# Kernel optimization log

Measured on AMD Instinct MI355X. Metric: run time of the kernel, lower is better.

## Reference

```python
import jax, jax.numpy as jnp
import numpy as np

B, N, F_IN, K, NUM_CLASSES = 16, 2048, 8, 35, 4
EPS = 1e-5


def _bn(x, g, b):
    # BatchNorm in training mode: stats over all leading (batch/node/edge) dims.
    ax = tuple(range(x.ndim - 1))
    mu = jnp.mean(x, axis=ax, keepdims=True)
    var = jnp.var(x, axis=ax, keepdims=True)
    return g * (x - mu) * jax.lax.rsqrt(var + EPS) + b


def _edge_feats(h, k):
    # h: [B,N,C]. Dynamic kNN within each graph (self included, as torch_cluster.knn),
    # then EdgeConv features cat([x_i, x_j - x_i]) -> [B,N,k,2C].
    sq = jnp.sum(h * h, -1)                                   # [B,N]
    d = sq[:, :, None] + sq[:, None, :] - 2.0 * jnp.einsum('bnc,bmc->bnm', h, h)
    _, idx = jax.lax.top_k(-d, k)                             # [B,N,k]
    hj = jax.vmap(lambda hb, ib: hb[ib])(h, idx)              # [B,N,k,C]
    hi = jnp.broadcast_to(h[:, :, None, :], hj.shape)
    return jnp.concatenate([hi, hj - hi], axis=-1)


def _forward(x, w1, b1, g1, bt1, w2, b2, g2, bt2, w3, b3, w4, b4,
             w5, b5, w6, b6, g6, bt6, w7, b7, g7, bt7, w8, b8):
    # conv1: DynamicEdgeConv(MLP([16,64,64,64]), k, 'max'); plain_last => 3rd linear bare
    e = _edge_feats(x, K)                                     # [B,N,K,16]
    h = jax.nn.relu(_bn(e @ w1 + b1, g1, bt1))
    h = jax.nn.relu(_bn(h @ w2 + b2, g2, bt2))
    h = h @ w3 + b3
    x1 = jnp.max(h, axis=2)                                   # [B,N,64] scatter-max over k
    # conv2: DynamicEdgeConv(MLP([128,128]), k, 'max'); single plain linear
    e2 = _edge_feats(x1, K)                                   # [B,N,K,128]
    x2 = jnp.max(e2 @ w4 + b4, axis=2)                        # [B,N,128]
    out = jnp.concatenate([x1, x2], axis=-1) @ w5 + b5        # [B,N,256]
    pooled = jnp.max(out, axis=1)                             # [B,256] global_max_pool
    # head MLP([256,128,64,4], dropout eval-mode, batch_norm), plain_last
    h = jax.nn.relu(_bn(pooled @ w6 + b6, g6, bt6))
    h = jax.nn.relu(_bn(h @ w7 + b7, g7, bt7))
    return h @ w8 + b8                                        # [B,4]


def setup_inputs() -> dict:
    key = jax.random.key(0)
    ks = jax.random.split(key, 12)

    def lin(kk, fi, fo):
        k1, k2 = jax.random.split(kk)
        w = jax.random.normal(k1, (fi, fo), jnp.float32) / np.sqrt(fi).astype(np.float32)
        b = jax.random.normal(k2, (fo,), jnp.float32) * 0.01
        return w, b

    x = jax.random.normal(ks[0], (B, N, F_IN), jnp.float32)
    w1, b1 = lin(ks[1], 2 * F_IN, 64)
    w2, b2 = lin(ks[2], 64, 64)
    w3, b3 = lin(ks[3], 64, 64)
    w4, b4 = lin(ks[4], 2 * 64, 128)
    w5, b5 = lin(ks[5], 128 + 64, 256)
    w6, b6 = lin(ks[6], 256, 128)
    w7, b7 = lin(ks[7], 128, 64)
    w8, b8 = lin(ks[8], 64, NUM_CLASSES)
    ones, zeros = jnp.ones, jnp.zeros
    return {
        'x': x,
        'w1': w1, 'b1': b1, 'g1': ones(64), 'bt1': zeros(64),
        'w2': w2, 'b2': b2, 'g2': ones(64), 'bt2': zeros(64),
        'w3': w3, 'b3': b3,
        'w4': w4, 'b4': b4,
        'w5': w5, 'b5': b5,
        'w6': w6, 'b6': b6, 'g6': ones(128), 'bt6': zeros(128),
        'w7': w7, 'b7': b7, 'g7': ones(64), 'bt7': zeros(64),
        'w8': w8, 'b8': b8,
    }


def reference(x, w1, b1, g1, bt1, w2, b2, g2, bt2, w3, b3, w4, b4,
              w5, b5, w6, b6, g6, bt6, w7, b7, g7, bt7, w8, b8):
    return _forward(x, w1, b1, g1, bt1, w2, b2, g2, bt2, w3, b3, w4, b4,
                    w5, b5, w6, b6, g6, bt6, w7, b7, g7, bt7, w8, b8)
```

## Files before the change

kernel.cpp:

```cpp
#include <hip/hip_runtime.h>
#include <cfloat>
#include <cstdint>

constexpr int Bn   = 16;
constexpr int Nn   = 2048;
constexpr int Fin  = 8;
constexpr int Kn   = 35;
constexpr int NODES = Bn * Nn;
constexpr int EDG   = NODES * Kn;
constexpr int NSTATB = 1024;
constexpr float EPSV = 1e-5f;

typedef _Float16 f16;
typedef _Float16 f16x2 __attribute__((ext_vector_type(2)));

__device__ __forceinline__ unsigned enc_f(float f){
    unsigned u = __float_as_uint(f);
    return (u & 0x80000000u) ? ~u : (u | 0x80000000u);
}
__device__ __forceinline__ float dec_f(unsigned e){
    unsigned u = (e & 0x80000000u) ? (e ^ 0x80000000u) : ~e;
    return __uint_as_float(u);
}

template<int C>
__global__ __launch_bounds__(256) void sq_kernel(const float* __restrict__ h, float* __restrict__ sq){
    int i = blockIdx.x * 256 + threadIdx.x;
    if (i >= NODES) return;
    const float* p = h + (size_t)i * C;
    float s = 0.f;
#pragma unroll
    for (int c = 0; c < C; c++) s += p[c] * p[c];
    sq[i] = s;
}

template<int C>
__global__ __launch_bounds__(256) void knn_kernel(const float* __restrict__ h, const float* __restrict__ sq,
                                                  int* __restrict__ idxout){
    __shared__ float dist[4][Nn];
    __shared__ float hi4[4][C];
    __shared__ float sqi[4];
    __shared__ float statred[4][3][4];
    __shared__ unsigned long long keybuf[4][128];
    int t  = threadIdx.x;
    int b  = blockIdx.x >> 9;
    int i0 = (blockIdx.x & 511) * 4;
    int w  = t >> 6, lane = t & 63;

    for (int i = t; i < 4 * C; i += 256)
        hi4[i / C][i % C] = h[((size_t)(b * Nn) + i0 + i / C) * C + (i % C)];
    if (t < 4) sqi[t] = sq[b * Nn + i0 + t];
    __syncthreads();

    const float4* H0 = (const float4*)hi4[0];
    const float4* H1 = (const float4*)hi4[1];
    const float4* H2 = (const float4*)hi4[2];
    const float4* H3 = (const float4*)hi4[3];
    float ps0=0.f,ps1=0.f,ps2=0.f,ps3=0.f, pq0=0.f,pq1=0.f,pq2=0.f,pq3=0.f;
    float mn0=FLT_MAX,mn1=FLT_MAX,mn2=FLT_MAX,mn3=FLT_MAX;
    for (int j = t; j < Nn; j += 256){
        const float4* hj = (const float4*)(h + ((size_t)(b * Nn) + j) * C);
        float d0 = 0.f, d1 = 0.f, d2 = 0.f, d3 = 0.f;
#pragma unroll 4
        for (int c4 = 0; c4 < C / 4; c4++){
            float4 v = hj[c4];
            float4 a0 = H0[c4], a1 = H1[c4], a2 = H2[c4], a3 = H3[c4];
            d0 += a0.x*v.x + a0.y*v.y + a0.z*v.z + a0.w*v.w;
            d1 += a1.x*v.x + a1.y*v.y + a1.z*v.z + a1.w*v.w;
            d2 += a2.x*v.x + a2.y*v.y + a2.z*v.z + a2.w*v.w;
            d3 += a3.x*v.x + a3.y*v.y + a3.z*v.z + a3.w*v.w;
        }
        float sj = sq[b * Nn + j];
        float D0 = sqi[0] + sj - 2.f*d0; dist[0][j] = D0; ps0 += D0; pq0 += D0*D0; mn0 = fminf(mn0, D0);
        float D1 = sqi[1] + sj - 2.f*d1; dist[1][j] = D1; ps1 += D1; pq1 += D1*D1; mn1 = fminf(mn1, D1);
        float D2 = sqi[2] + sj - 2.f*d2; dist[2][j] = D2; ps2 += D2; pq2 += D2*D2; mn2 = fminf(mn2, D2);
        float D3 = sqi[3] + sj - 2.f*d3; dist[3][j] = D3; ps3 += D3; pq3 += D3*D3; mn3 = fminf(mn3, D3);
    }
#pragma unroll
    for (int d = 1; d < 64; d <<= 1){
        ps0 += __shfl_xor(ps0, d); pq0 += __shfl_xor(pq0, d); mn0 = fminf(mn0, __shfl_xor(mn0, d));
        ps1 += __shfl_xor(ps1, d); pq1 += __shfl_xor(pq1, d); mn1 = fminf(mn1, __shfl_xor(mn1, d));
        ps2 += __shfl_xor(ps2, d); pq2 += __shfl_xor(pq2, d); mn2 = fminf(mn2, __shfl_xor(mn2, d));
        ps3 += __shfl_xor(ps3, d); pq3 += __shfl_xor(pq3, d); mn3 = fminf(mn3, __shfl_xor(mn3, d));
    }
    if (lane == 0){
        statred[0][0][w] = ps0; statred[0][1][w] = pq0; statred[0][2][w] = mn0;
        statred[1][0][w] = ps1; statred[1][1][w] = pq1; statred[1][2][w] = mn1;
        statred[2][0][w] = ps2; statred[2][1][w] = pq2; statred[2][2][w] = mn2;
        statred[3][0][w] = ps3; statred[3][1][w] = pq3; statred[3][2][w] = mn3;
    }
    __syncthreads();

    const float* dw = dist[w];
    float smu = statred[w][0][0] + statred[w][0][1] + statred[w][0][2] + statred[w][0][3];
    float mnq = fminf(fminf(statred[w][2][0], statred[w][2][1]),
                      fminf(statred[w][2][2], statred[w][2][3]));
    float mu = smu * (1.f / (float)Nn);
    float span = fmaxf(mu - mnq, 0.f);

    float lo = mnq;  int clo = 0;
    float hi = FLT_MAX;  int chi = Nn;

    float PV[5] = { mnq + 0.25f*span, mnq + 0.40f*span, mnq + 0.55f*span,
                    mnq + 0.75f*span, mu };
    int c0 = 0, c1 = 0, c2 = 0, c3 = 0, c4 = 0;
    for (int s8 = 0; s8 < 32; s8 += 8){
        float vv[8];
#pragma unroll
        for (int u = 0; u < 8; u++) vv[u] = dw[(s8 + u) * 64 + lane];
#pragma unroll
        for (int u = 0; u < 8; u++){
            float v = vv[u];
            c0 += (v < PV[0]) ? 1 : 0;
            c1 += (v < PV[1]) ? 1 : 0;
            c2 += (v < PV[2]) ? 1 : 0;
            c3 += (v < PV[3]) ? 1 : 0;
            c4 += (v < PV[4]) ? 1 : 0;
        }
    }
#pragma unroll
    for (int d = 1; d < 64; d <<= 1){
        c0 += __shfl_xor(c0, d);
        c1 += __shfl_xor(c1, d);
        c2 += __shfl_xor(c2, d);
        c3 += __shfl_xor(c3, d);
        c4 += __shfl_xor(c4, d);
    }
    {
        int CC[5] = {c0, c1, c2, c3, c4};
#pragma unroll
        for (int pi = 0; pi < 5; pi++){
            if (CC[pi] >= Kn){ if (PV[pi] < hi){ hi = PV[pi]; chi = CC[pi]; } }
            else             { if (PV[pi] > lo){ lo = PV[pi]; clo = CC[pi]; } }
        }
    }

    for (int it = 0; it < 24 && chi > 128; it++){
        int den = (chi - clo) > 0 ? (chi - clo) : 1;
        float piv = (it & 1) ? 0.5f * (lo + hi)
                             : lo + (hi - lo) * ((float)(96 - clo) / (float)den);
        if (!(piv > lo && piv < hi)) piv = 0.5f * (lo + hi);
        if (!(piv > lo && piv < hi)) break;
        int c = 0;
        for (int s8 = 0; s8 < 32; s8 += 8){
            float vv[8];
#pragma unroll
            for (int u = 0; u < 8; u++) vv[u] = dw[(s8 + u) * 64 + lane];
#pragma unroll
            for (int u = 0; u < 8; u++) c += (vv[u] < piv) ? 1 : 0;
        }
#pragma unroll
        for (int d = 1; d < 64; d <<= 1) c += __shfl_xor(c, d);
        if (c >= Kn){ hi = piv; chi = c; } else { lo = piv; clo = c; }
    }

    size_t obase = ((size_t)(b * Nn) + i0 + w) * Kn;

    if (chi <= 128){
        keybuf[w][lane]      = ~0ull;
        keybuf[w][lane + 64] = ~0ull;
        unsigned long long me_lower = (1ull << lane) - 1ull;
        int boff = 0;
        for (int s8 = 0; s8 < 32; s8 += 8){
            float vv[8];
#pragma unroll
            for (int u = 0; u < 8; u++) vv[u] = dw[(s8 + u) * 64 + lane];
#pragma unroll
            for (int u = 0; u < 8; u++){
                bool cnd = vv[u] < hi;
                unsigned long long m = __ballot(cnd);
                if (cnd){
                    int o = boff + __popcll(m & me_lower);
                    keybuf[w][o] = (((unsigned long long)enc_f(vv[u])) << 16) | (unsigned)((s8 + u) * 64 + lane);
                }
                boff += __popcll(m);
            }
        }
        unsigned long long k0 = keybuf[w][lane];
        unsigned long long k1 = keybuf[w][lane + 64];
        int r0 = 0, r1 = 0;
        int nR = (chi + 7) & ~7;
        for (int j2 = 0; j2 < nR; j2 += 8){
            unsigned long long a0 = keybuf[w][j2+0], a1 = keybuf[w][j2+1];
            unsigned long long a2 = keybuf[w][j2+2], a3 = keybuf[w][j2+3];
            unsigned long long a4 = keybuf[w][j2+4], a5 = keybuf[w][j2+5];
            unsigned long long a6 = keybuf[w][j2+6], a7 = keybuf[w][j2+7];
            r0 += (a0<k0)+(a1<k0)+(a2<k0)+(a3<k0)+(a4<k0)+(a5<k0)+(a6<k0)+(a7<k0);
            r1 += (a0<k1)+(a1<k1)+(a2<k1)+(a3<k1)+(a4<k1)+(a5<k1)+(a6<k1)+(a7<k1);
        }
        if (lane < chi      && r0 < Kn) idxout[obase + r0] = (int)(k0 & 0xffffu);
        if (lane + 64 < chi && r1 < Kn) idxout[obase + r1] = (int)(k1 & 0xffffu);
    } else {
        unsigned selmask = 0u;
        for (int e = 0; e < Kn; e++){
            unsigned long long best = ~0ull;
#pragma unroll
            for (int s = 0; s < 32; s++){
                float v = dw[s * 64 + lane];
                if (v < hi && !((selmask >> s) & 1)){
                    unsigned long long key = (((unsigned long long)enc_f(v)) << 16) | (unsigned)(s * 64 + lane);
                    best = (key < best) ? key : best;
                }
            }
#pragma unroll
            for (int d = 1; d < 64; d <<= 1){
                unsigned long long ov = __shfl_xor(best, d);
                best = (ov < best) ? ov : best;
            }
            int jj = (int)(best & 0xffffu);
            if ((jj & 63) == lane) selmask |= 1u << (jj >> 6);
            if (lane == 0) idxout[obase + e] = jj;
        }
    }
}

__global__ __launch_bounds__(256) void pre1_kernel(const float* __restrict__ x,
        const float* __restrict__ w1, const float* __restrict__ b1,
        float* __restrict__ p, float* __restrict__ q){
    int t = threadIdx.x, w = t >> 6, c = t & 63;
    float wd[8], wb[8];
#pragma unroll
    for (int f = 0; f < 8; f++){
        float wbv = w1[(8 + f) * 64 + c];
        wb[f] = wbv;
        wd[f] = w1[f * 64 + c] - wbv;
    }
    float b1c = b1[c];
    int slot = blockIdx.x * 4 + w;
    for (int it = 0; it < 16; it++){
        int node = slot + it * 2048;
        const float* xp = x + (size_t)node * Fin;
        float pv = b1c, qv = 0.f;
#pragma unroll
        for (int f = 0; f < 8; f++){
            float xv = xp[f];
            pv += xv * wd[f]; qv += xv * wb[f];
        }
        p[(size_t)node * 64 + c] = pv;
        q[(size_t)node * 64 + c] = qv;
    }
}

__global__ __launch_bounds__(256) void stats1_kernel(const float* __restrict__ p, const float* __restrict__ q,
        const int* __restrict__ idx, float* __restrict__ sumP, float* __restrict__ ssqP){
    __shared__ float red[2][4][64];
    int t = threadIdx.x, w = t >> 6, c = t & 63;
    float s = 0.f, ss = 0.f;
    int slot = blockIdx.x * 4 + w;
    for (int it = 0; it < 8; it++){
        int node = slot + it * 4096;
        int b = node >> 11;
        float pc = p[(size_t)node * 64 + c];
        const int* ip = idx + (size_t)node * Kn;
        for (int k = 0; k < Kn; k++){
            int j = ip[k];
            float z = pc + q[((size_t)(b << 11) + j) * 64 + c];
            s += z; ss += z * z;
        }
    }
    red[0][w][c] = s; red[1][w][c] = ss;
    __syncthreads();
    if (w == 0){
        sumP[blockIdx.x * 64 + c] = red[0][0][c] + red[0][1][c] + red[0][2][c] + red[0][3][c];
        ssqP[blockIdx.x * 64 + c] = red[1][0][c] + red[1][1][c] + red[1][2][c] + red[1][3][c];
    }
}

__global__ void finalize_kernel(const float* __restrict__ sumP, const float* __restrict__ ssqP,
        const float* __restrict__ gg, const float* __restrict__ bt,
        float* __restrict__ scale, float* __restrict__ shift, float inv_count){
    int c = threadIdx.x;
    float s = 0.f, q = 0.f;
    for (int i = 0; i < NSTATB; i++){ s += sumP[i * 64 + c]; q += ssqP[i * 64 + c]; }
    float mu  = s * inv_count;
    float var = q * inv_count - mu * mu;
    float sc  = gg[c] / sqrtf(var + EPSV);
    scale[c] = sc;
    shift[c] = bt[c] - mu * sc;
}

__global__ __launch_bounds__(256) void stats2_kernel(const float* __restrict__ p, const float* __restrict__ q,
        const int* __restrict__ idx,
        const float* __restrict__ sc1v, const float* __restrict__ sh1v,
        const float* __restrict__ w2, const float* __restrict__ b2,
        float* __restrict__ sumP, float* __restrict__ ssqP){
    __shared__ __align__(16) f16 hsh[4][2][64];
    __shared__ float red[2][4][64];
    int t = threadIdx.x, w = t >> 6, c = t & 63;
    f16x2 w2h[32];
#pragma unroll
    for (int f2 = 0; f2 < 32; f2++)
        w2h[f2] = f16x2{(f16)w2[(2*f2)*64 + c], (f16)w2[(2*f2+1)*64 + c]};
    float sc1 = sc1v[c], sh1 = sh1v[c], b2c = b2[c];
    float s = 0.f, ss = 0.f;
    int slot = blockIdx.x * 4 + w;
    for (int it = 0; it < 8; it++){
        int node = slot + it * 4096;
        int b = node >> 11;
        float pc = p[(size_t)node * 64 + c];
        const int* ip = idx + (size_t)node * Kn;
        for (int k = 0; k < Kn; k += 2){
            bool two = (k + 1 < Kn);
            int j0 = ip[k];
            int j1 = ip[two ? k + 1 : k];
            float za = pc + q[((size_t)(b << 11) + j0) * 64 + c];
            float zb = pc + q[((size_t)(b << 11) + j1) * 64 + c];
            hsh[w][0][c] = (f16)fmaxf(0.f, za * sc1 + sh1);
            hsh[w][1][c] = (f16)fmaxf(0.f, zb * sc1 + sh1);
            const uint4* h40 = (const uint4*)hsh[w][0];
            const uint4* h41 = (const uint4*)hsh[w][1];
            float p00=0.f,p01=0.f,p02=0.f,p03=0.f, p10=0.f,p11=0.f,p12=0.f,p13=0.f;
#pragma unroll
            for (int i = 0; i < 8; i++){
                uint4 u0 = h40[i], u1 = h41[i];
                p00 = __builtin_amdgcn_fdot2(__builtin_bit_cast(f16x2, u0.x), w2h[4*i+0], p00, false);
                p10 = __builtin_amdgcn_fdot2(__builtin_bit_cast(f16x2, u1.x), w2h[4*i+0], p10, false);
                p01 = __builtin_amdgcn_fdot2(__builtin_bit_cast(f16x2, u0.y), w2h[4*i+1], p01, false);
                p11 = __builtin_amdgcn_fdot2(__builtin_bit_cast(f16x2, u1.y), w2h[4*i+1], p11, false);
                p02 = __builtin_amdgcn_fdot2(__builtin_bit_cast(f16x2, u0.z), w2h[4*i+2], p02, false);
                p12 = __builtin_amdgcn_fdot2(__builtin_bit_cast(f16x2, u1.z), w2h[4*i+2], p12, false);
                p03 = __builtin_amdgcn_fdot2(__builtin_bit_cast(f16x2, u0.w), w2h[4*i+3], p03, false);
                p13 = __builtin_amdgcn_fdot2(__builtin_bit_cast(f16x2, u1.w), w2h[4*i+3], p13, false);
            }
            float z20 = b2c + ((p00 + p01) + (p02 + p03));
            float z21 = b2c + ((p10 + p11) + (p12 + p13));
            s += z20; ss += z20 * z20;
            if (two){ s += z21; ss += z21 * z21; }
        }
    }
    red[0][w][c] = s; red[1][w][c] = ss;
    __syncthreads();
    if (w == 0){
        sumP[blockIdx.x * 64 + c] = red[0][0][c] + red[0][1][c] + red[0][2][c] + red[0][3][c];
        ssqP[blockIdx.x * 64 + c] = red[1][0][c] + red[1][1][c] + red[1][2][c] + red[1][3][c];
    }
}

__global__ __launch_bounds__(256) void conv1_kernel(const float* __restrict__ p, const float* __restrict__ q,
        const int* __restrict__ idx,
        const float* __restrict__ sc1v, const float* __restrict__ sh1v,
        const float* __restrict__ w2, const float* __restrict__ b2,
        const float* __restrict__ sc2v, const float* __restrict__ sh2v,
        const float* __restrict__ w3, const float* __restrict__ b3,
        float* __restrict__ x1){
    __shared__ __align__(16) f16 hA[4][2][64];
    __shared__ __align__(16) f16 hB[4][2][64];
    int t = threadIdx.x, w = t >> 6, c = t & 63;
    f16x2 w2h[32], w3h[32];
#pragma unroll
    for (int f2 = 0; f2 < 32; f2++){
        w2h[f2] = f16x2{(f16)w2[(2*f2)*64 + c], (f16)w2[(2*f2+1)*64 + c]};
        w3h[f2] = f16x2{(f16)w3[(2*f2)*64 + c], (f16)w3[(2*f2+1)*64 + c]};
    }
    float sc1 = sc1v[c], sh1 = sh1v[c], sc2 = sc2v[c], sh2 = sh2v[c];
    float b2c = b2[c], b3c = b3[c];
    int node = blockIdx.x * 4 + w;
    int b = node >> 11;
    float pc = p[(size_t)node * 64 + c];
    const int* ip = idx + (size_t)node * Kn;
    float acc = -FLT_MAX;
    for (int k = 0; k < Kn; k += 2){
        bool two = (k + 1 < Kn);
        int j0 = ip[k];
        int j1 = ip[two ? k + 1 : k];
        float za = pc + q[((size_t)(b << 11) + j0) * 64 + c];
        float zb = pc + q[((size_t)(b << 11) + j1) * 64 + c];
        hA[w][0][c] = (f16)fmaxf(0.f, za * sc1 + sh1);
        hA[w][1][c] = (f16)fmaxf(0.f, zb * sc1 + sh1);
        const uint4* h40 = (const uint4*)hA[w][0];
        const uint4* h41 = (const uint4*)hA[w][1];
        float p00=0.f,p01=0.f,p02=0.f,p03=0.f, p10=0.f,p11=0.f,p12=0.f,p13=0.f;
#pragma unroll
        for (int i = 0; i < 8; i++){
            uint4 u0 = h40[i], u1 = h41[i];
            p00 = __builtin_amdgcn_fdot2(__builtin_bit_cast(f16x2, u0.x), w2h[4*i+0], p00, false);
            p10 = __builtin_amdgcn_fdot2(__builtin_bit_cast(f16x2, u1.x), w2h[4*i+0], p10, false);
            p01 = __builtin_amdgcn_fdot2(__builtin_bit_cast(f16x2, u0.y), w2h[4*i+1], p01, false);
            p11 = __builtin_amdgcn_fdot2(__builtin_bit_cast(f16x2, u1.y), w2h[4*i+1], p11, false);
            p02 = __builtin_amdgcn_fdot2(__builtin_bit_cast(f16x2, u0.z), w2h[4*i+2], p02, false);
            p12 = __builtin_amdgcn_fdot2(__builtin_bit_cast(f16x2, u1.z), w2h[4*i+2], p12, false);
            p03 = __builtin_amdgcn_fdot2(__builtin_bit_cast(f16x2, u0.w), w2h[4*i+3], p03, false);
            p13 = __builtin_amdgcn_fdot2(__builtin_bit_cast(f16x2, u1.w), w2h[4*i+3], p13, false);
        }
        float z20 = b2c + ((p00 + p01) + (p02 + p03));
        float z21 = b2c + ((p10 + p11) + (p12 + p13));
        hB[w][0][c] = (f16)fmaxf(0.f, z20 * sc2 + sh2);
        hB[w][1][c] = (f16)fmaxf(0.f, z21 * sc2 + sh2);
        const uint4* g40 = (const uint4*)hB[w][0];
        const uint4* g41 = (const uint4*)hB[w][1];
        float q00=0.f,q01=0.f,q02=0.f,q03=0.f, q10=0.f,q11=0.f,q12=0.f,q13=0.f;
#pragma unroll
        for (int i = 0; i < 8; i++){
            uint4 u0 = g40[i], u1 = g41[i];
            q00 = __builtin_amdgcn_fdot2(__builtin_bit_cast(f16x2, u0.x), w3h[4*i+0], q00, false);
            q10 = __builtin_amdgcn_fdot2(__builtin_bit_cast(f16x2, u1.x), w3h[4*i+0], q10, false);
            q01 = __builtin_amdgcn_fdot2(__builtin_bit_cast(f16x2, u0.y), w3h[4*i+1], q01, false);
            q11 = __builtin_amdgcn_fdot2(__builtin_bit_cast(f16x2, u1.y), w3h[4*i+1], q11, false);
            q02 = __builtin_amdgcn_fdot2(__builtin_bit_cast(f16x2, u0.z), w3h[4*i+2], q02, false);
            q12 = __builtin_amdgcn_fdot2(__builtin_bit_cast(f16x2, u1.z), w3h[4*i+2], q12, false);
            q03 = __builtin_amdgcn_fdot2(__builtin_bit_cast(f16x2, u0.w), w3h[4*i+3], q03, false);
            q13 = __builtin_amdgcn_fdot2(__builtin_bit_cast(f16x2, u1.w), w3h[4*i+3], q13, false);
        }
        float z30 = b3c + ((q00 + q01) + (q02 + q03));
        float z31 = b3c + ((q10 + q11) + (q12 + q13));
        acc = fmaxf(acc, z30);
        if (two) acc = fmaxf(acc, z31);
    }
    x1[(size_t)node * 64 + c] = acc;
}

__global__ __launch_bounds__(256) void pre2_kernel(const float* __restrict__ x1,
        const float* __restrict__ w4, const float* __restrict__ b4,
        float* __restrict__ u, float* __restrict__ v){
    __shared__ float x1s[16][64];
    int t = threadIdx.x;
    int c = t & 127, h = t >> 7;
    float wd[64], wb[64];
#pragma unroll
    for (int f = 0; f < 64; f++){
        float wbv = w4[(64 + f) * 128 + c];
        wb[f] = wbv;
        wd[f] = w4[f * 128 + c] - wbv;
    }
    float b4c = b4[c];
    int base = blockIdx.x * 16;
    for (int i = t; i < 16 * 64; i += 256)
        x1s[i >> 6][i & 63] = x1[(size_t)(base + (i >> 6)) * 64 + (i & 63)];
    __syncthreads();
    for (int n = 0; n < 8; n++){
        int node = base + h * 8 + n;
        const float4* xr = (const float4*)x1s[h * 8 + n];
        float u0 = 0.f, u1 = 0.f, v0 = 0.f, v1 = 0.f;
#pragma unroll
        for (int f4 = 0; f4 < 16; f4++){
            float4 xv = xr[f4];
            float pa = xv.x * wd[4*f4] + xv.y * wd[4*f4+1] + xv.z * wd[4*f4+2] + xv.w * wd[4*f4+3];
            float pb = xv.x * wb[4*f4] + xv.y * wb[4*f4+1] + xv.z * wb[4*f4+2] + xv.w * wb[4*f4+3];
            if (f4 & 1){ u1 += pa; v1 += pb; } else { u0 += pa; v0 += pb; }
        }
        u[(size_t)node * 128 + c] = b4c + u0 + u1;
        v[(size_t)node * 128 + c] = v0 + v1;
    }
}

__global__ __launch_bounds__(256) void gmax2_kernel(const float* __restrict__ v, const int* __restrict__ idx,
        float* __restrict__ x2){
    int t = threadIdx.x, g = t >> 7, c = t & 127;
    int node = blockIdx.x * 2 + g;
    int b = node >> 11;
    const int* ip = idx + (size_t)node * Kn;
    float vm = -FLT_MAX;
    for (int k = 0; k < Kn; k++){
        int j = ip[k];
        vm = fmaxf(vm, v[((size_t)(b << 11) + j) * 128 + c]);
    }
    x2[(size_t)node * 128 + c] += vm;
}

__global__ __launch_bounds__(256) void outpool_kernel(const float* __restrict__ x1, const float* __restrict__ x2,
        const float* __restrict__ w5, const float* __restrict__ b5, unsigned* __restrict__ pooled){
    __shared__ float rows[8][192];
    int t = threadIdx.x;
    int node0 = blockIdx.x * 8;
    for (int i = t; i < 8 * 192; i += 256){
        int e = i / 192, f = i - e * 192;
        int nd = node0 + e;
        rows[e][f] = (f < 64) ? x1[(size_t)nd * 64 + f] : x2[(size_t)nd * 128 + f - 64];
    }
    __syncthreads();
    float z[8];
#pragma unroll
    for (int e = 0; e < 8; e++) z[e] = b5[t];
    for (int f = 0; f < 192; f++){
        float w = w5[f * 256 + t];
#pragma unroll
        for (int e = 0; e < 8; e++) z[e] += rows[e][f] * w;
    }
    float m = z[0];
#pragma unroll
    for (int e = 1; e < 8; e++) m = fmaxf(m, z[e]);
    int b = node0 >> 11;
    atomicMax(&pooled[b * 256 + t], enc_f(m));
}

__global__ __launch_bounds__(256) void head_kernel(const unsigned* __restrict__ pooledE,
        const float* __restrict__ w6, const float* __restrict__ b6, const float* __restrict__ g6, const float* __restrict__ bt6,
        const float* __restrict__ w7, const float* __restrict__ b7, const float* __restrict__ g7, const float* __restrict__ bt7,
        const float* __restrict__ w8, const float* __restrict__ b8, float* __restrict__ out){
    __shared__ float P[16][256];
    __shared__ float H6[16][128];
    __shared__ float H7[16][64];
    int t = threadIdx.x;
    for (int i = t; i < 16 * 256; i += 256) P[i >> 8][i & 255] = dec_f(pooledE[i]);
    __syncthreads();
    for (int i = t; i < 16 * 128; i += 256){
        int r = i >> 7, c = i & 127;
        float z = b6[c];
        for (int f = 0; f < 256; f++) z += P[r][f] * w6[f * 128 + c];
        H6[r][c] = z;
    }
    __syncthreads();
    if (t < 128){
        float s = 0.f, q = 0.f;
        for (int r = 0; r < 16; r++){ float v = H6[r][t]; s += v; q += v * v; }
        float mu = s * (1.f / 16.f);
        float var = q * (1.f / 16.f) - mu * mu;
        float sc = g6[t] / sqrtf(var + EPSV);
        float sh = bt6[t] - mu * sc;
        for (int r = 0; r < 16; r++) H6[r][t] = fmaxf(0.f, H6[r][t] * sc + sh);
    }
    __syncthreads();
    for (int i = t; i < 16 * 64; i += 256){
        int r = i >> 6, c = i & 63;
        float z = b7[c];
        for (int f = 0; f < 128; f++) z += H6[r][f] * w7[f * 64 + c];
        H7[r][c] = z;
    }
    __syncthreads();
    if (t < 64){
        float s = 0.f, q = 0.f;
        for (int r = 0; r < 16; r++){ float v = H7[r][t]; s += v; q += v * v; }
        float mu = s * (1.f / 16.f);
        float var = q * (1.f / 16.f) - mu * mu;
        float sc = g7[t] / sqrtf(var + EPSV);
        float sh = bt7[t] - mu * sc;
        for (int r = 0; r < 16; r++) H7[r][t] = fmaxf(0.f, H7[r][t] * sc + sh);
    }
    __syncthreads();
    if (t < 64){
        int r = t >> 2, c = t & 3;
        float z = b8[c];
        for (int f = 0; f < 64; f++) z += H7[r][f] * w8[f * 4 + c];
        out[t] = z;
    }
}

extern "C" void kernel_launch(void* const* d_in, const int* in_sizes, int n_in,
                              void* d_out, int out_size, void* d_ws, size_t ws_size,
                              hipStream_t stream){
    const float* x   = (const float*)d_in[0];
    const float* w1  = (const float*)d_in[1];
    const float* b1  = (const float*)d_in[2];
    const float* g1  = (const float*)d_in[3];
    const float* bt1 = (const float*)d_in[4];
    const float* w2  = (const float*)d_in[5];
    const float* b2  = (const float*)d_in[6];
    const float* g2  = (const float*)d_in[7];
    const float* bt2 = (const float*)d_in[8];
    const float* w3  = (const float*)d_in[9];
    const float* b3  = (const float*)d_in[10];
    const float* w4  = (const float*)d_in[11];
    const float* b4  = (const float*)d_in[12];
    const float* w5  = (const float*)d_in[13];
    const float* b5  = (const float*)d_in[14];
    const float* w6  = (const float*)d_in[15];
    const float* b6  = (const float*)d_in[16];
    const float* g6  = (const float*)d_in[17];
    const float* bt6 = (const float*)d_in[18];
    const float* w7  = (const float*)d_in[19];
    const float* b7  = (const float*)d_in[20];
    const float* g7  = (const float*)d_in[21];
    const float* bt7 = (const float*)d_in[22];
    const float* w8  = (const float*)d_in[23];
    const float* b8  = (const float*)d_in[24];
    float* out = (float*)d_out;

    char* ws = (char*)d_ws;
    size_t off = 0;
    auto alloc = [&](size_t bytes)->char*{
        char* p = ws + off;
        off += (bytes + 255) & ~(size_t)255;
        return p;
    };
    int*      idx1   = (int*)alloc((size_t)EDG * 4);
    int*      idx2   = (int*)alloc((size_t)EDG * 4);
    float*    sq1    = (float*)alloc((size_t)NODES * 4);
    float*    sq2    = (float*)alloc((size_t)NODES * 4);
    float*    x1     = (float*)alloc((size_t)NODES * 64 * 4);
    float*    x2     = (float*)alloc((size_t)NODES * 128 * 4);
    float*    sumP   = (float*)alloc((size_t)NSTATB * 64 * 4);
    float*    ssqP   = (float*)alloc((size_t)NSTATB * 64 * 4);
    float*    scale1 = (float*)alloc(64 * 4);
    float*    shift1 = (float*)alloc(64 * 4);
    float*    scale2 = (float*)alloc(64 * 4);
    float*    shift2 = (float*)alloc(64 * 4);
    unsigned* pooled = (unsigned*)alloc((size_t)Bn * 256 * 4);
    float*    p      = (float*)alloc((size_t)NODES * 64 * 4);
    float*    q      = (float*)alloc((size_t)NODES * 64 * 4);
    float*    v      = p;

    hipMemsetAsync(pooled, 0, (size_t)Bn * 256 * 4, stream);

    sq_kernel<8><<<(NODES + 255) / 256, 256, 0, stream>>>(x, sq1);
    knn_kernel<8><<<NODES / 4, 256, 0, stream>>>(x, sq1, idx1);
    pre1_kernel<<<512, 256, 0, stream>>>(x, w1, b1, p, q);
    stats1_kernel<<<NSTATB, 256, 0, stream>>>(p, q, idx1, sumP, ssqP);
    finalize_kernel<<<1, 64, 0, stream>>>(sumP, ssqP, g1, bt1, scale1, shift1, 1.0f / (float)EDG);
    stats2_kernel<<<NSTATB, 256, 0, stream>>>(p, q, idx1, scale1, shift1, w2, b2, sumP, ssqP);
    finalize_kernel<<<1, 64, 0, stream>>>(sumP, ssqP, g2, bt2, scale2, shift2, 1.0f / (float)EDG);
    conv1_kernel<<<NODES / 4, 256, 0, stream>>>(p, q, idx1, scale1, shift1,
                                                w2, b2, scale2, shift2, w3, b3, x1);
    sq_kernel<64><<<(NODES + 255) / 256, 256, 0, stream>>>(x1, sq2);
    knn_kernel<64><<<NODES / 4, 256, 0, stream>>>(x1, sq2, idx2);
    pre2_kernel<<<NODES / 16, 256, 0, stream>>>(x1, w4, b4, x2, v);
    gmax2_kernel<<<NODES / 2, 256, 0, stream>>>(v, idx2, x2);
    outpool_kernel<<<NODES / 8, 256, 0, stream>>>(x1, x2, w5, b5, pooled);
    head_kernel<<<1, 256, 0, stream>>>(pooled, w6, b6, g6, bt6, w7, b7, g7, bt7, w8, b8, out);
}
```

Before: 1.335 ms.

## Split each kNN query row across two wavefronts with 512-thread blocks

After: 1.387 ms. 1.04x slower.

```diff
diff --git a/kernel.cpp b/kernel.cpp
--- a/kernel.cpp
+++ b/kernel.cpp
@@ -35,19 +35,20 @@
 }
 
 template<int C>
-__global__ __launch_bounds__(256) void knn_kernel(const float* __restrict__ h, const float* __restrict__ sq,
+__global__ __launch_bounds__(512) void knn_kernel(const float* __restrict__ h, const float* __restrict__ sq,
                                                   int* __restrict__ idxout){
     __shared__ float dist[4][Nn];
     __shared__ float hi4[4][C];
     __shared__ float sqi[4];
-    __shared__ float statred[4][3][4];
+    __shared__ float statred[4][3][8];
+    __shared__ int   cntred[4][6][2];
     __shared__ unsigned long long keybuf[4][128];
     int t  = threadIdx.x;
     int b  = blockIdx.x >> 9;
     int i0 = (blockIdx.x & 511) * 4;
     int w  = t >> 6, lane = t & 63;
 
-    for (int i = t; i < 4 * C; i += 256)
+    for (int i = t; i < 4 * C; i += 512)
         hi4[i / C][i % C] = h[((size_t)(b * Nn) + i0 + i / C) * C + (i % C)];
     if (t < 4) sqi[t] = sq[b * Nn + i0 + t];
     __syncthreads();
@@ -58,7 +59,7 @@
     const float4* H3 = (const float4*)hi4[3];
     float ps0=0.f,ps1=0.f,ps2=0.f,ps3=0.f, pq0=0.f,pq1=0.f,pq2=0.f,pq3=0.f;
     float mn0=FLT_MAX,mn1=FLT_MAX,mn2=FLT_MAX,mn3=FLT_MAX;
-    for (int j = t; j < Nn; j += 256){
+    for (int j = t; j < Nn; j += 512){
         const float4* hj = (const float4*)(h + ((size_t)(b * Nn) + j) * C);
         float d0 = 0.f, d1 = 0.f, d2 = 0.f, d3 = 0.f;
 #pragma unroll 4
@@ -91,10 +92,13 @@
     }
     __syncthreads();
 
-    const float* dw = dist[w];
-    float smu = statred[w][0][0] + statred[w][0][1] + statred[w][0][2] + statred[w][0][3];
-    float mnq = fminf(fminf(statred[w][2][0], statred[w][2][1]),
-                      fminf(statred[w][2][2], statred[w][2][3]));
+    int qq = w >> 1, half = w & 1;
+    const float* dw = dist[qq];
+    int s0 = half * 16;
+
+    float smu = 0.f, mnq = FLT_MAX;
+#pragma unroll
+    for (int i = 0; i < 8; i++){ smu += statred[qq][0][i]; mnq = fminf(mnq, statred[qq][2][i]); }
     float mu = smu * (1.f / (float)Nn);
     float span = fmaxf(mu - mnq, 0.f);
 
@@ -103,31 +107,40 @@
 
     float PV[5] = { mnq + 0.25f*span, mnq + 0.40f*span, mnq + 0.55f*span,
                     mnq + 0.75f*span, mu };
-    int c0 = 0, c1 = 0, c2 = 0, c3 = 0, c4 = 0;
-    for (int s8 = 0; s8 < 32; s8 += 8){
-        float vv[8];
-#pragma unroll
-        for (int u = 0; u < 8; u++) vv[u] = dw[(s8 + u) * 64 + lane];
-#pragma unroll
-        for (int u = 0; u < 8; u++){
-            float v = vv[u];
-            c0 += (v < PV[0]) ? 1 : 0;
-            c1 += (v < PV[1]) ? 1 : 0;
-            c2 += (v < PV[2]) ? 1 : 0;
-            c3 += (v < PV[3]) ? 1 : 0;
-            c4 += (v < PV[4]) ? 1 : 0;
-        }
-    }
-#pragma unroll
-    for (int d = 1; d < 64; d <<= 1){
-        c0 += __shfl_xor(c0, d);
-        c1 += __shfl_xor(c1, d);
-        c2 += __shfl_xor(c2, d);
-        c3 += __shfl_xor(c3, d);
-        c4 += __shfl_xor(c4, d);
-    }
     {
-        int CC[5] = {c0, c1, c2, c3, c4};
+        int c0 = 0, c1 = 0, c2 = 0, c3 = 0, c4 = 0;
+        for (int s8 = s0; s8 < s0 + 16; s8 += 8){
+            float vv[8];
+#pragma unroll
+            for (int u = 0; u < 8; u++) vv[u] = dw[(s8 + u) * 64 + lane];
+#pragma unroll
+            for (int u = 0; u < 8; u++){
+                float v = vv[u];
+                c0 += (v < PV[0]) ? 1 : 0;
+                c1 += (v < PV[1]) ? 1 : 0;
+                c2 += (v < PV[2]) ? 1 : 0;
+                c3 += (v < PV[3]) ? 1 : 0;
+                c4 += (v < PV[4]) ? 1 : 0;
+            }
+        }
+#pragma unroll
+        for (int d = 1; d < 64; d <<= 1){
+            c0 += __shfl_xor(c0, d);
+            c1 += __shfl_xor(c1, d);
+            c2 += __shfl_xor(c2, d);
+            c3 += __shfl_xor(c3, d);
+            c4 += __shfl_xor(c4, d);
+        }
+        if (lane == 0){
+            cntred[qq][0][half] = c0; cntred[qq][1][half] = c1; cntred[qq][2][half] = c2;
+            cntred[qq][3][half] = c3; cntred[qq][4][half] = c4;
+        }
+    }
+    __syncthreads();
+    {
+        int CC[5];
+#pragma unroll
+        for (int pi = 0; pi < 5; pi++) CC[pi] = cntred[qq][pi][0] + cntred[qq][pi][1];
 #pragma unroll
         for (int pi = 0; pi < 5; pi++){
             if (CC[pi] >= Kn){ if (PV[pi] < hi){ hi = PV[pi]; chi = CC[pi]; } }
@@ -135,62 +148,95 @@
         }
     }
 
-    for (int it = 0; it < 24 && chi > 128; it++){
-        int den = (chi - clo) > 0 ? (chi - clo) : 1;
-        float piv = (it & 1) ? 0.5f * (lo + hi)
-                             : lo + (hi - lo) * ((float)(96 - clo) / (float)den);
-        if (!(piv > lo && piv < hi)) piv = 0.5f * (lo + hi);
-        if (!(piv > lo && piv < hi)) break;
+    for (int it = 0; it < 4; it++){
+        bool act = (chi > 128);
+        float piv = 0.f;
         int c = 0;
-        for (int s8 = 0; s8 < 32; s8 += 8){
-            float vv[8];
-#pragma unroll
-            for (int u = 0; u < 8; u++) vv[u] = dw[(s8 + u) * 64 + lane];
-#pragma unroll
-            for (int u = 0; u < 8; u++) c += (vv[u] < piv) ? 1 : 0;
-        }
-#pragma unroll
-        for (int d = 1; d < 64; d <<= 1) c += __shfl_xor(c, d);
-        if (c >= Kn){ hi = piv; chi = c; } else { lo = piv; clo = c; }
-    }
-
-    size_t obase = ((size_t)(b * Nn) + i0 + w) * Kn;
-
-    if (chi <= 128){
-        keybuf[w][lane]      = ~0ull;
-        keybuf[w][lane + 64] = ~0ull;
-        unsigned long long me_lower = (1ull << lane) - 1ull;
-        int boff = 0;
-        for (int s8 = 0; s8 < 32; s8 += 8){
-            float vv[8];
-#pragma unroll
-            for (int u = 0; u < 8; u++) vv[u] = dw[(s8 + u) * 64 + lane];
-#pragma unroll
-            for (int u = 0; u < 8; u++){
-                bool cnd = vv[u] < hi;
-                unsigned long long m = __ballot(cnd);
-                if (cnd){
-                    int o = boff + __popcll(m & me_lower);
-                    keybuf[w][o] = (((unsigned long long)enc_f(vv[u])) << 16) | (unsigned)((s8 + u) * 64 + lane);
+        if (act){
+            int den = (chi - clo) > 0 ? (chi - clo) : 1;
+            piv = (it & 1) ? 0.5f * (lo + hi)
+                           : lo + (hi - lo) * ((float)(96 - clo) / (float)den);
+            if (!(piv > lo && piv < hi)) piv = 0.5f * (lo + hi);
+            if (piv > lo && piv < hi){
+                for (int s8 = s0; s8 < s0 + 16; s8 += 8){
+                    float vv[8];
+#pragma unroll
+                    for (int u = 0; u < 8; u++) vv[u] = dw[(s8 + u) * 64 + lane];
+#pragma unroll
+                    for (int u = 0; u < 8; u++) c += (vv[u] < piv) ? 1 : 0;
                 }
-                boff += __popcll(m);
+#pragma unroll
+                for (int d = 1; d < 64; d <<= 1) c += __shfl_xor(c, d);
+            } else act = false;
+        }
+        __syncthreads();
+        if (lane == 0) cntred[qq][5][half] = c;
+        __syncthreads();
+        if (act){
+            int ct = cntred[qq][5][0] + cntred[qq][5][1];
+            if (ct >= Kn){ if (piv < hi){ hi = piv; chi = ct; } }
+            else         { if (piv > lo){ lo = piv; clo = ct; } }
+        }
+    }
+
+    size_t obase = ((size_t)(b * Nn) + i0 + qq) * Kn;
+    bool ok = (chi <= 128);
+    unsigned long long me_lower = (1ull << lane) - 1ull;
+
+    {
+        int ch = 0;
+        if (ok){
+            for (int s8 = s0; s8 < s0 + 16; s8 += 8){
+                float vv[8];
+#pragma unroll
+                for (int u = 0; u < 8; u++) vv[u] = dw[(s8 + u) * 64 + lane];
+#pragma unroll
+                for (int u = 0; u < 8; u++) ch += (vv[u] < hi) ? 1 : 0;
             }
-        }
-        unsigned long long k0 = keybuf[w][lane];
-        unsigned long long k1 = keybuf[w][lane + 64];
-        int r0 = 0, r1 = 0;
+#pragma unroll
+            for (int d = 1; d < 64; d <<= 1) ch += __shfl_xor(ch, d);
+        }
+        __syncthreads();
+        if (lane == 0) cntred[qq][5][half] = ch;
+        keybuf[qq][half * 64 + lane] = ~0ull;
+        __syncthreads();
+    }
+    {
+        int boff = (half == 1) ? cntred[qq][5][0] : 0;
+        if (ok){
+            for (int s8 = s0; s8 < s0 + 16; s8 += 8){
+                float vv[8];
+#pragma unroll
+                for (int u = 0; u < 8; u++) vv[u] = dw[(s8 + u) * 64 + lane];
+#pragma unroll
+                for (int u = 0; u < 8; u++){
+                    bool cnd = vv[u] < hi;
+                    unsigned long long m = __ballot(cnd);
+                    if (cnd){
+                        int o = boff + __popcll(m & me_lower);
+                        if (o < 128)
+                            keybuf[qq][o] = (((unsigned long long)enc_f(vv[u])) << 16) | (unsigned)((s8 + u) * 64 + lane);
+                    }
+                    boff += __popcll(m);
+                }
+            }
+        }
+        __syncthreads();
+    }
+    if (ok){
+        int pos = half * 64 + lane;
+        unsigned long long k0 = keybuf[qq][pos];
+        int r0 = 0;
         int nR = (chi + 7) & ~7;
         for (int j2 = 0; j2 < nR; j2 += 8){
-            unsigned long long a0 = keybuf[w][j2+0], a1 = keybuf[w][j2+1];
-            unsigned long long a2 = keybuf[w][j2+2], a3 = keybuf[w][j2+3];
-            unsigned long long a4 = keybuf[w][j2+4], a5 = keybuf[w][j2+5];
-            unsigned long long a6 = keybuf[w][j2+6], a7 = keybuf[w][j2+7];
+            unsigned long long a0 = keybuf[qq][j2+0], a1 = keybuf[qq][j2+1];
+            unsigned long long a2 = keybuf[qq][j2+2], a3 = keybuf[qq][j2+3];
+            unsigned long long a4 = keybuf[qq][j2+4], a5 = keybuf[qq][j2+5];
+            unsigned long long a6 = keybuf[qq][j2+6], a7 = keybuf[qq][j2+7];
             r0 += (a0<k0)+(a1<k0)+(a2<k0)+(a3<k0)+(a4<k0)+(a5<k0)+(a6<k0)+(a7<k0);
-            r1 += (a0<k1)+(a1<k1)+(a2<k1)+(a3<k1)+(a4<k1)+(a5<k1)+(a6<k1)+(a7<k1);
-        }
-        if (lane < chi      && r0 < Kn) idxout[obase + r0] = (int)(k0 & 0xffffu);
-        if (lane + 64 < chi && r1 < Kn) idxout[obase + r1] = (int)(k1 & 0xffffu);
-    } else {
+        }
+        if (pos < chi && r0 < Kn) idxout[obase + r0] = (int)(k0 & 0xffffu);
+    } else if (half == 0){
         unsigned selmask = 0u;
         for (int e = 0; e < Kn; e++){
             unsigned long long best = ~0ull;
@@ -592,7 +638,7 @@
     hipMemsetAsync(pooled, 0, (size_t)Bn * 256 * 4, stream);
 
     sq_kernel<8><<<(NODES + 255) / 256, 256, 0, stream>>>(x, sq1);
-    knn_kernel<8><<<NODES / 4, 256, 0, stream>>>(x, sq1, idx1);
+    knn_kernel<8><<<NODES / 4, 512, 0, stream>>>(x, sq1, idx1);
     pre1_kernel<<<512, 256, 0, stream>>>(x, w1, b1, p, q);
     stats1_kernel<<<NSTATB, 256, 0, stream>>>(p, q, idx1, sumP, ssqP);
     finalize_kernel<<<1, 64, 0, stream>>>(sumP, ssqP, g1, bt1, scale1, shift1, 1.0f / (float)EDG);
@@ -601,7 +647,7 @@
     conv1_kernel<<<NODES / 4, 256, 0, stream>>>(p, q, idx1, scale1, shift1,
                                                 w2, b2, scale2, shift2, w3, b3, x1);
     sq_kernel<64><<<(NODES + 255) / 256, 256, 0, stream>>>(x1, sq2);
-    knn_kernel<64><<<NODES / 4, 256, 0, stream>>>(x1, sq2, idx2);
+    knn_kernel<64><<<NODES / 4, 512, 0, stream>>>(x1, sq2, idx2);
     pre2_kernel<<<NODES / 16, 256, 0, stream>>>(x1, w4, b4, x2, v);
     gmax2_kernel<<<NODES / 2, 256, 0, stream>>>(v, idx2, x2);
     outpool_kernel<<<NODES / 8, 256, 0, stream>>>(x1, x2, w5, b5, pooled);
```
